# Kernel tuning notes

Measured on AMD Instinct MI355X. Metric: run time of the kernel, lower is better.

Reference implementation:

```python
import jax, jax.numpy as jnp
import numpy as np

B, T, V, D, U = 256, 1024, 6, 64, 64  # batch, seq, vocab, embed dim, lstm units


def _lstm_dir(x_seq, mask_seq, Wk, Wr, b, reverse):
    # x_seq: [B,T,D], mask_seq: [B,T] bool. Keras gate order: i, f, g(cell), o.
    Bc, Tc, _ = x_seq.shape
    Uc = Wr.shape[0]
    if reverse:
        x_seq = x_seq[:, ::-1, :]
        mask_seq = mask_seq[:, ::-1]
    # precompute input projections for all timesteps (one big GEMM)
    xproj = jnp.einsum('btd,dg->tbg', x_seq, Wk) + b          # [T,B,4U]
    m = jnp.swapaxes(mask_seq, 0, 1)[..., None]               # [T,B,1]

    def step(carry, inp):
        h, c = carry
        xp, mt = inp
        z = xp + h @ Wr                                        # [B,4U]
        i, f, g, o = jnp.split(z, 4, axis=-1)
        i = jax.nn.sigmoid(i)
        f = jax.nn.sigmoid(f)
        g = jnp.tanh(g)
        o = jax.nn.sigmoid(o)
        c_new = f * c + i * g
        h_new = o * jnp.tanh(c_new)
        # masked steps carry state through and repeat previous output
        h = jnp.where(mt, h_new, h)
        c = jnp.where(mt, c_new, c)
        return (h, c), h

    h0 = jnp.zeros((Bc, Uc), x_seq.dtype)
    _, ys = jax.lax.scan(step, (h0, h0), (xproj, m))           # ys: [T,B,U]
    ys = jnp.swapaxes(ys, 0, 1)                                # [B,T,U]
    if reverse:
        ys = ys[:, ::-1, :]
    return ys


def reference(tokens, emb, Wk_f, Wr_f, b_f, Wk_b, Wr_b, b_b, Wd, bd):
    x = emb[tokens]                                            # [B,T,D]
    mask = jnp.any(x != 0, axis=-1)                            # Masking(0): all-zero feature vec -> masked
    y_f = _lstm_dir(x, mask, Wk_f, Wr_f, b_f, reverse=False)   # [B,T,U]
    y_b = _lstm_dir(x, mask, Wk_b, Wr_b, b_b, reverse=True)    # [B,T,U]
    y = jnp.concatenate([y_f, y_b], axis=-1)                   # [B,T,2U]
    last = y[:, -1, :]                                         # [B,2U]
    return last @ Wd + bd                                      # [B,1]


def setup_inputs() -> dict:
    key = jax.random.key(0)
    ks = jax.random.split(key, 8)
    return {
        'tokens': jax.random.randint(ks[0], (B, T), 0, V, dtype=jnp.int32),
        'emb': jax.random.normal(ks[1], (V, D), dtype=jnp.float32),
        'Wk_f': jax.random.normal(ks[2], (D, 4 * U), dtype=jnp.float32) * 0.05,
        'Wr_f': jax.random.normal(ks[3], (U, 4 * U), dtype=jnp.float32) * 0.05,
        'b_f': jnp.zeros((4 * U,), dtype=jnp.float32),
        'Wk_b': jax.random.normal(ks[4], (D, 4 * U), dtype=jnp.float32) * 0.05,
        'Wr_b': jax.random.normal(ks[5], (U, 4 * U), dtype=jnp.float32) * 0.05,
        'b_b': jnp.zeros((4 * U,), dtype=jnp.float32),
        'Wd': jax.random.normal(ks[6], (2 * U, 1), dtype=jnp.float32) * 0.05,
        'bd': jnp.zeros((1,), dtype=jnp.float32),
    }
```

## Files before the change

### kernel.cpp

```cpp
#include <hip/hip_runtime.h>


constexpr int kB = 256;
constexpr int kT = 1024;
constexpr int kV = 6;
constexpr int kD = 64;
constexpr int kU = 64;
constexpr int kG = 256;

#define LOG2E 1.44269504f

typedef _Float16 v2h __attribute__((ext_vector_type(2)));

__device__ __forceinline__ float fast_rcp(float x) { return __builtin_amdgcn_rcpf(x); }
__device__ __forceinline__ float exp2_f(float x)   { return __builtin_amdgcn_exp2f(x); }
__device__ __forceinline__ float sig_f(float z)  { return fast_rcp(1.0f + exp2_f(-LOG2E * z)); }
__device__ __forceinline__ float tanh_f(float z) { return 2.0f * fast_rcp(1.0f + exp2_f(-2.0f * LOG2E * z)) - 1.0f; }

__device__ __forceinline__ v2h as_v2h(float x) { return __builtin_bit_cast(v2h, x); }

__global__ __launch_bounds__(256)
__attribute__((amdgpu_waves_per_eu(1, 1)))
void bilstm_last_kernel(
    const int*   __restrict__ tokens,
    const float* __restrict__ emb,
    const float* __restrict__ Wk_f,
    const float* __restrict__ Wr_f,
    const float* __restrict__ b_f,
    const float* __restrict__ Wk_b,
    const float* __restrict__ b_b,
    const float* __restrict__ Wd,
    const float* __restrict__ bd,
    float*       __restrict__ out)
{
    __shared__ float s_emb[kV * kD];
    __shared__ float __align__(16) s_proj[kV * kG];
    __shared__ int   __align__(16) s_tok[kT];
    __shared__ _Float16 __align__(16) s_hh[4][kU];
    __shared__ float s_act[2][kG];

    const int b   = blockIdx.x;
    const int tid = threadIdx.x;
    const int l   = tid & 63;
    const int g   = tid >> 6;

    for (int i = tid; i < kV * kD; i += 256) s_emb[i] = emb[i];
    ((int4*)s_tok)[tid] = ((const int4*)(tokens + b * kT))[tid];
    s_hh[g][l] = (_Float16)0.f;
    __syncthreads();

    unsigned int mbv = 0;
#pragma unroll
    for (int v = 0; v < kV; ++v) {
        const unsigned long long bb = __ballot(s_emb[v * kD + l] != 0.0f);
        mbv |= (bb != 0ull) ? (1u << v) : 0u;
    }
    const unsigned int smb = __builtin_amdgcn_readfirstlane(mbv);

    const int tokL = __builtin_amdgcn_readfirstlane(s_tok[kT - 1]);

    float afv[kV];
    float ab;
    {
        const float bf = b_f[tid];
#pragma unroll
        for (int v = 0; v < kV; ++v) afv[v] = bf;
        ab = b_b[tid];
#pragma unroll 4
        for (int d = 0; d < kD; ++d) {
            const float wkf = Wk_f[d * kG + tid];
            const float wkb = Wk_b[d * kG + tid];
            afv[0] = fmaf(s_emb[0 * kD + d], wkf, afv[0]);
            afv[1] = fmaf(s_emb[1 * kD + d], wkf, afv[1]);
            afv[2] = fmaf(s_emb[2 * kD + d], wkf, afv[2]);
            afv[3] = fmaf(s_emb[3 * kD + d], wkf, afv[3]);
            afv[4] = fmaf(s_emb[4 * kD + d], wkf, afv[4]);
            afv[5] = fmaf(s_emb[5 * kD + d], wkf, afv[5]);
            ab     = fmaf(s_emb[tokL * kD + d], wkb, ab);
        }
#pragma unroll
        for (int v = 0; v < kV; ++v) s_proj[v * kG + tid] = afv[v];
    }

    {
        const float abact = (g == 2) ? tanh_f(ab) : sig_f(ab);
        s_act[1][tid] = abact;
    }
    __syncthreads();

    float hb_val;
    {
        const float ib = s_act[1][0 * kU + l];
        const float gb = s_act[1][2 * kU + l];
        const float ob = s_act[1][3 * kU + l];
        const float cb = ib * gb;
        const float hb = ob * tanh_f(cb);
        hb_val = ((smb >> tokL) & 1) ? hb : 0.0f;
    }

#define DECLW(p)                                                              \
    v2h wh_##p;                                                               \
    wh_##p.x = (_Float16)Wr_f[(2 * (p) + 0) * kG + tid];                      \
    wh_##p.y = (_Float16)Wr_f[(2 * (p) + 1) * kG + tid];
    DECLW(0)  DECLW(1)  DECLW(2)  DECLW(3)  DECLW(4)  DECLW(5)  DECLW(6)  DECLW(7)
    DECLW(8)  DECLW(9)  DECLW(10) DECLW(11) DECLW(12) DECLW(13) DECLW(14) DECLW(15)
    DECLW(16) DECLW(17) DECLW(18) DECLW(19) DECLW(20) DECLW(21) DECLW(22) DECLW(23)
    DECLW(24) DECLW(25) DECLW(26) DECLW(27) DECLW(28) DECLW(29) DECLW(30) DECLW(31)
#undef DECLW

    const float aScale = (g == 2) ? -2.0f * LOG2E : -LOG2E;
    const float aMul   = (g == 2) ? 2.0f : 1.0f;
    const float aAdd   = (g == 2) ? -1.0f : 0.0f;

    float c = 0.0f, hreg = 0.0f;

    int stok0 = __builtin_amdgcn_readfirstlane(s_tok[0]);
    float zcur = s_proj[stok0 * kG + tid];
    int mskc = (smb >> stok0) & 1;
    int stokA = __builtin_amdgcn_readfirstlane(s_tok[1]);

#define STEP(P, TT)                                                           \
    {                                                                         \
           \
        const float4* hp = (const float4*)s_hh[g];                            \
        const float4 hv0 = hp[0], hv1 = hp[1], hv2 = hp[2], hv3 = hp[3];      \
        const float4 hv4 = hp[4], hv5 = hp[5], hv6 = hp[6], hv7 = hp[7];      \
        const int   vtokB = s_tok[((TT) + 2) & (kT - 1)];                     \
        const float znext = s_proj[stokA * kG + tid];                         \
        const int   mskn  = (int)((smb >> stokA) & 1);                        \
        const v2h H0  = as_v2h(hv0.x), H1  = as_v2h(hv0.y);                   \
        const v2h H2  = as_v2h(hv0.z), H3  = as_v2h(hv0.w);                   \
        const v2h H4  = as_v2h(hv1.x), H5  = as_v2h(hv1.y);                   \
        const v2h H6  = as_v2h(hv1.z), H7  = as_v2h(hv1.w);                   \
        const v2h H8  = as_v2h(hv2.x), H9  = as_v2h(hv2.y);                   \
        const v2h H10 = as_v2h(hv2.z), H11 = as_v2h(hv2.w);                   \
        const v2h H12 = as_v2h(hv3.x), H13 = as_v2h(hv3.y);                   \
        const v2h H14 = as_v2h(hv3.z), H15 = as_v2h(hv3.w);                   \
        const v2h H16 = as_v2h(hv4.x), H17 = as_v2h(hv4.y);                   \
        const v2h H18 = as_v2h(hv4.z), H19 = as_v2h(hv4.w);                   \
        const v2h H20 = as_v2h(hv5.x), H21 = as_v2h(hv5.y);                   \
        const v2h H22 = as_v2h(hv5.z), H23 = as_v2h(hv5.w);                   \
        const v2h H24 = as_v2h(hv6.x), H25 = as_v2h(hv6.y);                   \
        const v2h H26 = as_v2h(hv6.z), H27 = as_v2h(hv6.w);                   \
        const v2h H28 = as_v2h(hv7.x), H29 = as_v2h(hv7.y);                   \
        const v2h H30 = as_v2h(hv7.z), H31 = as_v2h(hv7.w);                   \
               \
        float pa = __builtin_amdgcn_fdot2(H0,  wh_0,  zcur, false);           \
        float pb = __builtin_amdgcn_fdot2(H1,  wh_1,  0.0f, false);           \
        pa = __builtin_amdgcn_fdot2(H2,  wh_2,  pa, false);                   \
        pb = __builtin_amdgcn_fdot2(H3,  wh_3,  pb, false);                   \
        pa = __builtin_amdgcn_fdot2(H4,  wh_4,  pa, false);                   \
        pb = __builtin_amdgcn_fdot2(H5,  wh_5,  pb, false);                   \
        pa = __builtin_amdgcn_fdot2(H6,  wh_6,  pa, false);                   \
        pb = __builtin_amdgcn_fdot2(H7,  wh_7,  pb, false);                   \
        pa = __builtin_amdgcn_fdot2(H8,  wh_8,  pa, false);                   \
        pb = __builtin_amdgcn_fdot2(H9,  wh_9,  pb, false);                   \
        pa = __builtin_amdgcn_fdot2(H10, wh_10, pa, false);                   \
        pb = __builtin_amdgcn_fdot2(H11, wh_11, pb, false);                   \
        pa = __builtin_amdgcn_fdot2(H12, wh_12, pa, false);                   \
        pb = __builtin_amdgcn_fdot2(H13, wh_13, pb, false);                   \
        pa = __builtin_amdgcn_fdot2(H14, wh_14, pa, false);                   \
        pb = __builtin_amdgcn_fdot2(H15, wh_15, pb, false);                   \
        pa = __builtin_amdgcn_fdot2(H16, wh_16, pa, false);                   \
        pb = __builtin_amdgcn_fdot2(H17, wh_17, pb, false);                   \
        pa = __builtin_amdgcn_fdot2(H18, wh_18, pa, false);                   \
        pb = __builtin_amdgcn_fdot2(H19, wh_19, pb, false);                   \
        pa = __builtin_amdgcn_fdot2(H20, wh_20, pa, false);                   \
        pb = __builtin_amdgcn_fdot2(H21, wh_21, pb, false);                   \
        pa = __builtin_amdgcn_fdot2(H22, wh_22, pa, false);                   \
        pb = __builtin_amdgcn_fdot2(H23, wh_23, pb, false);                   \
        pa = __builtin_amdgcn_fdot2(H24, wh_24, pa, false);                   \
        pb = __builtin_amdgcn_fdot2(H25, wh_25, pb, false);                   \
        pa = __builtin_amdgcn_fdot2(H26, wh_26, pa, false);                   \
        pb = __builtin_amdgcn_fdot2(H27, wh_27, pb, false);                   \
        pa = __builtin_amdgcn_fdot2(H28, wh_28, pa, false);                   \
        pb = __builtin_amdgcn_fdot2(H29, wh_29, pb, false);                   \
        pa = __builtin_amdgcn_fdot2(H30, wh_30, pa, false);                   \
        pb = __builtin_amdgcn_fdot2(H31, wh_31, pb, false);                   \
        const float z = pa + pb;                                              \
                            \
        const float e = exp2_f(z * aScale);                                   \
        const float r = fast_rcp(1.0f + e);                                   \
        const float a = fmaf(r, aMul, aAdd);                                  \
        s_act[P][tid] = a;                                                    \
        __syncthreads();                                                      \
        const float ai  = s_act[P][0 * kU + l];                               \
        const float af_ = s_act[P][1 * kU + l];                               \
        const float ag  = s_act[P][2 * kU + l];                               \
        const float ao  = s_act[P][3 * kU + l];                               \
        const float cn = fmaf(af_, c, ai * ag);                               \
        const float hn = ao * tanh_f(cn);                                     \
        if (mskc) { c = cn; hreg = hn; }                  \
        s_hh[g][l] = (_Float16)hreg;                                          \
        zcur = znext; mskc = mskn;                                            \
        stokA = __builtin_amdgcn_readfirstlane(vtokB);                        \
    }

#pragma unroll 1
    for (int t = 0; t < kT; t += 2) {
        STEP(0, t)
        STEP(1, t + 1)
    }
#undef STEP

    if (tid < kU) {
        float v = hreg * Wd[tid] + hb_val * Wd[kU + tid];
#pragma unroll
        for (int off = 32; off > 0; off >>= 1) v += __shfl_down(v, off, 64);
        if (tid == 0) out[b] = v + bd[0];
    }
}

extern "C" void kernel_launch(void* const* d_in, const int* in_sizes, int n_in,
                              void* d_out, int out_size, void* d_ws, size_t ws_size,
                              hipStream_t stream) {
    const int*   tokens = (const int*)d_in[0];
    const float* emb    = (const float*)d_in[1];
    const float* Wk_f   = (const float*)d_in[2];
    const float* Wr_f   = (const float*)d_in[3];
    const float* b_f    = (const float*)d_in[4];
    const float* Wk_b   = (const float*)d_in[5];
    const float* b_b    = (const float*)d_in[7];
    const float* Wd     = (const float*)d_in[8];
    const float* bd     = (const float*)d_in[9];
    float* out = (float*)d_out;

    bilstm_last_kernel<<<kB, 256, 0, stream>>>(
        tokens, emb, Wk_f, Wr_f, b_f, Wk_b, b_b, Wd, bd, out);
}
```

Measured before the change: 405.5 us.

## Interleave gate columns per unit and exchange activations via DPP broadcasts

Columns are remapped so the four gates of one hidden unit sit in four adjacent lanes. The gate activations are then gathered with DPP quad broadcasts instead of a shared-memory round trip, which removes one of the two per-step barriers. The hidden state is double-buffered so a single sync per step is enough. The fdot2 chain is also split into four accumulators to shorten the dependency chain, and the final dot product now reduces across all four waves.

```diff
diff --git a/kernel.cpp b/kernel.cpp
--- a/kernel.cpp
+++ b/kernel.cpp
@@ -11,6 +11,13 @@
 #define LOG2E 1.44269504f
 
 typedef _Float16 v2h __attribute__((ext_vector_type(2)));
+
+template <int CTRL>
+__device__ __forceinline__ float dppf(float x) {
+    return __int_as_float(
+        __builtin_amdgcn_mov_dpp(__float_as_int(x), CTRL, 0xF, 0xF, true));
+}
+constexpr int kBc0 = 0x00, kBc1 = 0x55, kBc2 = 0xAA, kBc3 = 0xFF;
 
 __device__ __forceinline__ float fast_rcp(float x) { return __builtin_amdgcn_rcpf(x); }
 __device__ __forceinline__ float exp2_f(float x)   { return __builtin_amdgcn_exp2f(x); }
@@ -34,19 +41,23 @@
     float*       __restrict__ out)
 {
     __shared__ float s_emb[kV * kD];
-    __shared__ float __align__(16) s_proj[kV * kG];
+    __shared__ float __align__(16) s_projP[kV * kG];
     __shared__ int   __align__(16) s_tok[kT];
-    __shared__ _Float16 __align__(16) s_hh[4][kU];
-    __shared__ float s_act[2][kG];
+    __shared__ _Float16 __align__(16) s_hh[2][kU];
+    __shared__ float s_red[4];
 
     const int b   = blockIdx.x;
     const int tid = threadIdx.x;
     const int l   = tid & 63;
-    const int g   = tid >> 6;
+    const int wv  = tid >> 6;
+    const int s   = l & 3;
+    const int k   = l >> 2;
+    const int u   = wv * 16 + k;
+    const int col = s * kU + u;
 
     for (int i = tid; i < kV * kD; i += 256) s_emb[i] = emb[i];
     ((int4*)s_tok)[tid] = ((const int4*)(tokens + b * kT))[tid];
-    s_hh[g][l] = (_Float16)0.f;
+    if (tid < 2 * kU) ((_Float16*)s_hh)[tid] = (_Float16)0.f;
     __syncthreads();
 
     unsigned int mbv = 0;
@@ -59,17 +70,17 @@
 
     const int tokL = __builtin_amdgcn_readfirstlane(s_tok[kT - 1]);
 
-    float afv[kV];
     float ab;
     {
-        const float bf = b_f[tid];
+        float afv[kV];
+        const float bf = b_f[col];
 #pragma unroll
         for (int v = 0; v < kV; ++v) afv[v] = bf;
-        ab = b_b[tid];
+        ab = b_b[col];
 #pragma unroll 4
         for (int d = 0; d < kD; ++d) {
-            const float wkf = Wk_f[d * kG + tid];
-            const float wkb = Wk_b[d * kG + tid];
+            const float wkf = Wk_f[d * kG + col];
+            const float wkb = Wk_b[d * kG + col];
             afv[0] = fmaf(s_emb[0 * kD + d], wkf, afv[0]);
             afv[1] = fmaf(s_emb[1 * kD + d], wkf, afv[1]);
             afv[2] = fmaf(s_emb[2 * kD + d], wkf, afv[2]);
@@ -79,20 +90,22 @@
             ab     = fmaf(s_emb[tokL * kD + d], wkb, ab);
         }
 #pragma unroll
-        for (int v = 0; v < kV; ++v) s_proj[v * kG + tid] = afv[v];
-    }
-
-    {
-        const float abact = (g == 2) ? tanh_f(ab) : sig_f(ab);
-        s_act[1][tid] = abact;
-    }
-    __syncthreads();
+        for (int v = 0; v < kV; ++v) s_projP[v * kG + tid] = afv[v];
+    }
+
+    const bool  isg    = (s == 2);
+    const float aScale = isg ? -2.0f * LOG2E : -LOG2E;
+    const float aMul   = isg ? 2.0f : 1.0f;
+    const float aAdd   = isg ? -1.0f : 0.0f;
 
     float hb_val;
     {
-        const float ib = s_act[1][0 * kU + l];
-        const float gb = s_act[1][2 * kU + l];
-        const float ob = s_act[1][3 * kU + l];
+        const float e = exp2_f(ab * aScale);
+        const float r = fast_rcp(1.0f + e);
+        const float a = fmaf(r, aMul, aAdd);
+        const float ib = dppf<kBc0>(a);
+        const float gb = dppf<kBc2>(a);
+        const float ob = dppf<kBc3>(a);
         const float cb = ib * gb;
         const float hb = ob * tanh_f(cb);
         hb_val = ((smb >> tokL) & 1) ? hb : 0.0f;
@@ -100,33 +113,29 @@
 
 #define DECLW(p)                                                              \
     v2h wh_##p;                                                               \
-    wh_##p.x = (_Float16)Wr_f[(2 * (p) + 0) * kG + tid];                      \
-    wh_##p.y = (_Float16)Wr_f[(2 * (p) + 1) * kG + tid];
+    wh_##p.x = (_Float16)Wr_f[(2 * (p) + 0) * kG + col];                      \
+    wh_##p.y = (_Float16)Wr_f[(2 * (p) + 1) * kG + col];
     DECLW(0)  DECLW(1)  DECLW(2)  DECLW(3)  DECLW(4)  DECLW(5)  DECLW(6)  DECLW(7)
     DECLW(8)  DECLW(9)  DECLW(10) DECLW(11) DECLW(12) DECLW(13) DECLW(14) DECLW(15)
     DECLW(16) DECLW(17) DECLW(18) DECLW(19) DECLW(20) DECLW(21) DECLW(22) DECLW(23)
     DECLW(24) DECLW(25) DECLW(26) DECLW(27) DECLW(28) DECLW(29) DECLW(30) DECLW(31)
 #undef DECLW
 
-    const float aScale = (g == 2) ? -2.0f * LOG2E : -LOG2E;
-    const float aMul   = (g == 2) ? 2.0f : 1.0f;
-    const float aAdd   = (g == 2) ? -1.0f : 0.0f;
-
     float c = 0.0f, hreg = 0.0f;
 
     int stok0 = __builtin_amdgcn_readfirstlane(s_tok[0]);
-    float zcur = s_proj[stok0 * kG + tid];
+    float zcur = s_projP[stok0 * kG + tid];
     int mskc = (smb >> stok0) & 1;
     int stokA = __builtin_amdgcn_readfirstlane(s_tok[1]);
 
-#define STEP(P, TT)                                                           \
+#define STEP(RP, WP, TT)                                                      \
     {                                                                         \
-           \
-        const float4* hp = (const float4*)s_hh[g];                            \
+        const float4* hp = (const float4*)s_hh[RP];                           \
         const float4 hv0 = hp[0], hv1 = hp[1], hv2 = hp[2], hv3 = hp[3];      \
         const float4 hv4 = hp[4], hv5 = hp[5], hv6 = hp[6], hv7 = hp[7];      \
+                          \
         const int   vtokB = s_tok[((TT) + 2) & (kT - 1)];                     \
-        const float znext = s_proj[stokA * kG + tid];                         \
+        const float znext = s_projP[stokA * kG + tid];                        \
         const int   mskn  = (int)((smb >> stokA) & 1);                        \
         const v2h H0  = as_v2h(hv0.x), H1  = as_v2h(hv0.y);                   \
         const v2h H2  = as_v2h(hv0.z), H3  = as_v2h(hv0.w);                   \
@@ -144,71 +153,73 @@
         const v2h H26 = as_v2h(hv6.z), H27 = as_v2h(hv6.w);                   \
         const v2h H28 = as_v2h(hv7.x), H29 = as_v2h(hv7.y);                   \
         const v2h H30 = as_v2h(hv7.z), H31 = as_v2h(hv7.w);                   \
-               \
+                        \
         float pa = __builtin_amdgcn_fdot2(H0,  wh_0,  zcur, false);           \
         float pb = __builtin_amdgcn_fdot2(H1,  wh_1,  0.0f, false);           \
-        pa = __builtin_amdgcn_fdot2(H2,  wh_2,  pa, false);                   \
-        pb = __builtin_amdgcn_fdot2(H3,  wh_3,  pb, false);                   \
+        float pc = __builtin_amdgcn_fdot2(H2,  wh_2,  0.0f, false);           \
+        float pd = __builtin_amdgcn_fdot2(H3,  wh_3,  0.0f, false);           \
         pa = __builtin_amdgcn_fdot2(H4,  wh_4,  pa, false);                   \
         pb = __builtin_amdgcn_fdot2(H5,  wh_5,  pb, false);                   \
-        pa = __builtin_amdgcn_fdot2(H6,  wh_6,  pa, false);                   \
-        pb = __builtin_amdgcn_fdot2(H7,  wh_7,  pb, false);                   \
+        pc = __builtin_amdgcn_fdot2(H6,  wh_6,  pc, false);                   \
+        pd = __builtin_amdgcn_fdot2(H7,  wh_7,  pd, false);                   \
         pa = __builtin_amdgcn_fdot2(H8,  wh_8,  pa, false);                   \
         pb = __builtin_amdgcn_fdot2(H9,  wh_9,  pb, false);                   \
-        pa = __builtin_amdgcn_fdot2(H10, wh_10, pa, false);                   \
-        pb = __builtin_amdgcn_fdot2(H11, wh_11, pb, false);                   \
+        pc = __builtin_amdgcn_fdot2(H10, wh_10, pc, false);                   \
+        pd = __builtin_amdgcn_fdot2(H11, wh_11, pd, false);                   \
         pa = __builtin_amdgcn_fdot2(H12, wh_12, pa, false);                   \
         pb = __builtin_amdgcn_fdot2(H13, wh_13, pb, false);                   \
-        pa = __builtin_amdgcn_fdot2(H14, wh_14, pa, false);                   \
-        pb = __builtin_amdgcn_fdot2(H15, wh_15, pb, false);                   \
+        pc = __builtin_amdgcn_fdot2(H14, wh_14, pc, false);                   \
+        pd = __builtin_amdgcn_fdot2(H15, wh_15, pd, false);                   \
         pa = __builtin_amdgcn_fdot2(H16, wh_16, pa, false);                   \
         pb = __builtin_amdgcn_fdot2(H17, wh_17, pb, false);                   \
-        pa = __builtin_amdgcn_fdot2(H18, wh_18, pa, false);                   \
-        pb = __builtin_amdgcn_fdot2(H19, wh_19, pb, false);                   \
+        pc = __builtin_amdgcn_fdot2(H18, wh_18, pc, false);                   \
+        pd = __builtin_amdgcn_fdot2(H19, wh_19, pd, false);                   \
         pa = __builtin_amdgcn_fdot2(H20, wh_20, pa, false);                   \
         pb = __builtin_amdgcn_fdot2(H21, wh_21, pb, false);                   \
-        pa = __builtin_amdgcn_fdot2(H22, wh_22, pa, false);                   \
-        pb = __builtin_amdgcn_fdot2(H23, wh_23, pb, false);                   \
+        pc = __builtin_amdgcn_fdot2(H22, wh_22, pc, false);                   \
+        pd = __builtin_amdgcn_fdot2(H23, wh_23, pd, false);                   \
         pa = __builtin_amdgcn_fdot2(H24, wh_24, pa, false);                   \
         pb = __builtin_amdgcn_fdot2(H25, wh_25, pb, false);                   \
-        pa = __builtin_amdgcn_fdot2(H26, wh_26, pa, false);                   \
-        pb = __builtin_amdgcn_fdot2(H27, wh_27, pb, false);                   \
+        pc = __builtin_amdgcn_fdot2(H26, wh_26, pc, false);                   \
+        pd = __builtin_amdgcn_fdot2(H27, wh_27, pd, false);                   \
         pa = __builtin_amdgcn_fdot2(H28, wh_28, pa, false);                   \
         pb = __builtin_amdgcn_fdot2(H29, wh_29, pb, false);                   \
-        pa = __builtin_amdgcn_fdot2(H30, wh_30, pa, false);                   \
-        pb = __builtin_amdgcn_fdot2(H31, wh_31, pb, false);                   \
-        const float z = pa + pb;                                              \
-                            \
+        pc = __builtin_amdgcn_fdot2(H30, wh_30, pc, false);                   \
+        pd = __builtin_amdgcn_fdot2(H31, wh_31, pd, false);                   \
+        const float z = (pa + pb) + (pc + pd);                                \
+                                \
         const float e = exp2_f(z * aScale);                                   \
         const float r = fast_rcp(1.0f + e);                                   \
         const float a = fmaf(r, aMul, aAdd);                                  \
-        s_act[P][tid] = a;                                                    \
-        __syncthreads();                                                      \
-        const float ai  = s_act[P][0 * kU + l];                               \
-        const float af_ = s_act[P][1 * kU + l];                               \
-        const float ag  = s_act[P][2 * kU + l];                               \
-        const float ao  = s_act[P][3 * kU + l];                               \
-        const float cn = fmaf(af_, c, ai * ag);                               \
+                  \
+        const float ai = dppf<kBc0>(a);                                       \
+        const float af = dppf<kBc1>(a);                                       \
+        const float ag = dppf<kBc2>(a);                                       \
+        const float ao = dppf<kBc3>(a);                                       \
+        const float cn = fmaf(af, c, ai * ag);                                \
         const float hn = ao * tanh_f(cn);                                     \
         if (mskc) { c = cn; hreg = hn; }                  \
-        s_hh[g][l] = (_Float16)hreg;                                          \
+        if (s == 0) s_hh[WP][u] = (_Float16)hreg;                             \
+        __syncthreads();                                                      \
         zcur = znext; mskc = mskn;                                            \
         stokA = __builtin_amdgcn_readfirstlane(vtokB);                        \
     }
 
 #pragma unroll 1
     for (int t = 0; t < kT; t += 2) {
-        STEP(0, t)
-        STEP(1, t + 1)
+        STEP(0, 1, t)
+        STEP(1, 0, t + 1)
     }
 #undef STEP
 
-    if (tid < kU) {
-        float v = hreg * Wd[tid] + hb_val * Wd[kU + tid];
+    {
+        float v = (s == 0) ? (hreg * Wd[u] + hb_val * Wd[kU + u]) : 0.0f;
 #pragma unroll
         for (int off = 32; off > 0; off >>= 1) v += __shfl_down(v, off, 64);
-        if (tid == 0) out[b] = v + bd[0];
-    }
+        if (l == 0) s_red[wv] = v;
+    }
+    __syncthreads();
+    if (tid == 0) out[b] = (s_red[0] + s_red[1]) + (s_red[2] + s_red[3]) + bd[0];
 }
 
 extern "C" void kernel_launch(void* const* d_in, const int* in_sizes, int n_in,
```

Result: faster. 349.5 us (-13.8%).
